# Kernel optimization log

Hardware: AMD Instinct MI355X
Metric: run time of the kernel (lower is better)

Reference implementation:

```python
import jax, jax.numpy as jnp
import numpy as np

D = 512       # hidden_size (attention defaults hardcode 512)
N = 8         # num_heads
H = D // N    # depth per head = 64
FF = 2048     # FFN filter size (hardcoded)
EPS = 1e-6


def _layer_norm(x, gamma, beta):
    # matches functional layer_norm: biased variance, eps inside sqrt
    mean = jnp.mean(x, axis=-1, keepdims=True)
    var = jnp.mean((x - mean) ** 2, axis=-1, keepdims=True)
    return gamma * ((x - mean) / jnp.sqrt(var + EPS)) + beta


def setup_inputs() -> dict:
    key = jax.random.key(0)
    ks = jax.random.split(key, 12)
    B, S = 8, 1024
    s = lambda k, shape, scale: jax.random.normal(k, shape, jnp.float32) * scale
    return {
        "inputs": s(ks[0], (B, S, D), 1.0),
        "attention_bias": jnp.zeros((B, 1, 1, S), jnp.float32),
        "ln1_g": jnp.ones((D,), jnp.float32),
        "ln1_b": jnp.zeros((D,), jnp.float32),
        "wq": s(ks[1], (D, N, H), D ** -0.5),
        "wk": s(ks[2], (D, N, H), D ** -0.5),
        "wv": s(ks[3], (D, N, H), D ** -0.5),
        "wo": s(ks[4], (N, H, D), D ** -0.5),
        "ln2_g": jnp.ones((D,), jnp.float32),
        "ln2_b": jnp.zeros((D,), jnp.float32),
        "w1": s(ks[5], (D, FF), D ** -0.5),
        "b1": jnp.zeros((FF,), jnp.float32),
        "w2": s(ks[6], (FF, D), FF ** -0.5),
        "b2": jnp.zeros((D,), jnp.float32),
    }


def reference(inputs, attention_bias, ln1_g, ln1_b, wq, wk, wv, wo,
              ln2_g, ln2_b, w1, b1, w2, b2):
    # --- self-attention block (pre-LN, residual) ---
    y = _layer_norm(inputs, ln1_g, ln1_b)
    q = jnp.einsum('bsd,dnh->bsnh', y, wq) * (H ** -0.5)
    k = jnp.einsum('bsd,dnh->bsnh', y, wk)
    v = jnp.einsum('bsd,dnh->bsnh', y, wv)
    # logits[b,n,f,t] = sum_h k[b,t,n,h] * q[b,f,n,h]
    logits = jnp.einsum('btnh,bfnh->bnft', k, q) + attention_bias
    weights = jax.nn.softmax(logits, axis=3)
    attn = jnp.einsum('bnft,btnh->bfnh', weights, v)
    attn_out = jnp.einsum('bfnh,nhd->bfd', attn, wo)
    x = inputs + attn_out

    # --- FFN block (pre-LN, residual) ---
    y2 = _layer_norm(x, ln2_g, ln2_b)
    h = jax.nn.relu(jnp.einsum('bsd,df->bsf', y2, w1) + b1)
    ffn_out = jnp.einsum('bsf,fd->bsd', h, w2) + b2
    return x + ffn_out
```

## Files before the change

### kernel.cpp

```cpp
#include <hip/hip_runtime.h>
#include <stdint.h>

typedef unsigned short u16;
typedef __attribute__((ext_vector_type(8))) __bf16 bf16x8;
typedef __attribute__((ext_vector_type(2))) __bf16 bf16x2;
typedef __attribute__((ext_vector_type(4))) float f32x4;

__device__ __forceinline__ float bf2f(u16 u) {
    union { unsigned int i; float f; } c; c.i = ((unsigned int)u) << 16; return c.f;
}
__device__ __forceinline__ u16 f2bf_sw(float f) {
    union { float f; unsigned int i; } c; c.f = f;
    unsigned int u = c.i;
    u += 0x7FFFu + ((u >> 16) & 1u);
    return (u16)(u >> 16);
}
__device__ __forceinline__ unsigned f2bf2(float lo, float hi) {
#if __has_builtin(__builtin_amdgcn_cvt_pk_bf16_f32)
    union { bf16x2 v; unsigned u; } c;
    c.v = __builtin_amdgcn_cvt_pk_bf16_f32(lo, hi);
    return c.u;
#else
    return (unsigned)f2bf_sw(lo) | ((unsigned)f2bf_sw(hi) << 16);
#endif
}
__device__ __forceinline__ u16 f2bf(float f) {
#if __has_builtin(__builtin_amdgcn_cvt_pk_bf16_f32)
    return (u16)(f2bf2(f, 0.f) & 0xFFFFu);
#else
    return f2bf_sw(f);
#endif
}
__device__ __forceinline__ bool sniff_f32(const unsigned* probe) {
    return probe && ((*probe & 0xFFFFu) == 0u);
}
__device__ __forceinline__ float lde(const void* p, size_t i, bool isf32) {
    return isf32 ? ((const float*)p)[i] : bf2f(((const u16*)p)[i]);
}
__device__ __forceinline__ void g2lds16(const void* g, void* l) {
    __builtin_amdgcn_global_load_lds(
        (__attribute__((address_space(1))) void*)(uintptr_t)g,
        (__attribute__((address_space(3))) void*)(unsigned int)(uintptr_t)l,
        16, 0, 0);
}

__global__ void prep_weights(const void* __restrict__ wq, const void* __restrict__ wk,
                             const void* __restrict__ wv, const void* __restrict__ wo,
                             const void* __restrict__ w1, const void* __restrict__ w2,
                             u16* __restrict__ wqkvT, u16* __restrict__ woT,
                             u16* __restrict__ w1T, u16* __restrict__ w2T,
                             const unsigned* probe) {
    __shared__ u16 t[32][33];
    const bool isf32 = sniff_f32(probe);
    const int id = blockIdx.x;
    const void* src; u16* dst; int R, C, cb, rb; float scale = 1.f;
    if (id < 1024) {
        const int which = id >> 8, tl = id & 255;
        R = 512; C = 512; cb = (tl & 15) * 32; rb = (tl >> 4) * 32;
        if (which == 0)      { src = wq; dst = wqkvT;              scale = 0.18033688011112042f; }
        else if (which == 1) { src = wk; dst = wqkvT + 512 * 512; }
        else if (which == 2) { src = wv; dst = wqkvT + 1024 * 512; }
        else                 { src = wo; dst = woT; }
    } else if (id < 2048) {
        const int tl = id - 1024; src = w1; dst = w1T; R = 512; C = 2048;
        cb = (tl & 63) * 32; rb = (tl >> 6) * 32;
    } else {
        const int tl = id - 2048; src = w2; dst = w2T; R = 2048; C = 512;
        cb = (tl & 15) * 32; rb = (tl >> 4) * 32;
    }
    const int tx = threadIdx.x, ty = threadIdx.y;
#pragma unroll
    for (int i = 0; i < 4; i++)
        t[ty + i * 8][tx] = f2bf(lde(src, (size_t)(rb + ty + i * 8) * C + cb + tx, isf32));
    __syncthreads();
#pragma unroll
    for (int i = 0; i < 4; i++) {
        float v = bf2f(t[tx][ty + i * 8]) * scale;
        dst[(size_t)(cb + ty + i * 8) * R + rb + tx] = f2bf(v);
    }
}

__global__ __launch_bounds__(256) void ln_any(const void* __restrict__ x,
                                              const void* __restrict__ gw,
                                              const void* __restrict__ bw,
                                              u16* __restrict__ y,
                                              const unsigned* probe_x,
                                              const unsigned* probe_gb) {
    const bool xf32 = sniff_f32(probe_x);
    const bool gf32 = sniff_f32(probe_gb);
    const int lane = threadIdx.x & 63, wave = threadIdx.x >> 6;
    const int r = blockIdx.x * 4 + wave;
    union U8 { uint4 v; u16 s[8]; };
    float xs[8];
    if (xf32) {
        const float4* xr = (const float4*)((const float*)x + (size_t)r * 512 + lane * 8);
        float4 p0 = xr[0], p1 = xr[1];
        xs[0]=p0.x; xs[1]=p0.y; xs[2]=p0.z; xs[3]=p0.w;
        xs[4]=p1.x; xs[5]=p1.y; xs[6]=p1.z; xs[7]=p1.w;
    } else {
        U8 xu; xu.v = *(const uint4*)((const u16*)x + (size_t)r * 512 + lane * 8);
#pragma unroll
        for (int j = 0; j < 8; j++) xs[j] = bf2f(xu.s[j]);
    }
    float s1 = 0.f, s2 = 0.f;
#pragma unroll
    for (int j = 0; j < 8; j++) { s1 += xs[j]; s2 += xs[j] * xs[j]; }
#pragma unroll
    for (int d = 1; d < 64; d <<= 1) { s1 += __shfl_xor(s1, d); s2 += __shfl_xor(s2, d); }
    const float mean = s1 * (1.f / 512.f);
    const float var = s2 * (1.f / 512.f) - mean * mean;
    const float rstd = rsqrtf(var + 1e-6f);
    float gs[8], bs[8];
    if (gf32) {
        const float4* gr = (const float4*)((const float*)gw + lane * 8);
        const float4* br = (const float4*)((const float*)bw + lane * 8);
        float4 g0 = gr[0], g1 = gr[1], b0 = br[0], b1 = br[1];
        gs[0]=g0.x; gs[1]=g0.y; gs[2]=g0.z; gs[3]=g0.w; gs[4]=g1.x; gs[5]=g1.y; gs[6]=g1.z; gs[7]=g1.w;
        bs[0]=b0.x; bs[1]=b0.y; bs[2]=b0.z; bs[3]=b0.w; bs[4]=b1.x; bs[5]=b1.y; bs[6]=b1.z; bs[7]=b1.w;
    } else {
        U8 gu; gu.v = *(const uint4*)((const u16*)gw + lane * 8);
        U8 bu; bu.v = *(const uint4*)((const u16*)bw + lane * 8);
#pragma unroll
        for (int j = 0; j < 8; j++) { gs[j] = bf2f(gu.s[j]); bs[j] = bf2f(bu.s[j]); }
    }
    uint4 ov;
    float o[8];
#pragma unroll
    for (int j = 0; j < 8; j++) o[j] = gs[j] * ((xs[j] - mean) * rstd) + bs[j];
    ov.x = f2bf2(o[0], o[1]); ov.y = f2bf2(o[2], o[3]);
    ov.z = f2bf2(o[4], o[5]); ov.w = f2bf2(o[6], o[7]);
    *(uint4*)(y + (size_t)r * 512 + lane * 8) = ov;
}

template <int EPI, int TM>
__global__ __launch_bounds__(256, 2) void gemm_bt(const u16* __restrict__ A,
                                                  const u16* __restrict__ Bt,
                                                  const void* __restrict__ bias,
                                                  const void* __restrict__ res,
                                                  void* __restrict__ out,
                                                  u16* __restrict__ out2,
                                                  const unsigned* probe,
                                                  int M, int N, int K) {
    constexpr int ACH = TM / 16;
    constexpr int MI = TM / 32;
    __shared__ __align__(16) u16 lA[2][TM * 32];
    __shared__ __align__(16) u16 lB[2][128 * 32];
    const int tid = threadIdx.x, wave = tid >> 6, lane = tid & 63;
    const int m0 = blockIdx.x * TM, n0 = blockIdx.y * 128;
    const int wm = (wave >> 1) * (TM / 2), wn = (wave & 1) * 64;
    const int row = lane & 15, quad = lane >> 4;
    f32x4 acc[MI][4];
#pragma unroll
    for (int i = 0; i < MI; i++)
#pragma unroll
        for (int j = 0; j < 4; j++) acc[i][j] = (f32x4){0.f, 0.f, 0.f, 0.f};
    const u16* Ab = A + (size_t)m0 * K;
    const u16* Bb = Bt + (size_t)n0 * K;

    auto stage = [&](int buf, int k0) {
#pragma unroll
        for (int c = 0; c < (ACH + 8 + 3) / 4; c++) {
            const int ch = c * 4 + wave;
            if (ch < ACH) {
                const int e = ch * 64 + lane;
                const int r = e >> 2, col = (e & 3) * 8;
                g2lds16(Ab + (size_t)r * K + k0 + col, (char*)lA[buf] + ch * 1024);
            } else if (ch < ACH + 8) {
                const int c2 = ch - ACH;
                const int e = c2 * 64 + lane;
                const int r = e >> 2, col = (e & 3) * 8;
                g2lds16(Bb + (size_t)r * K + k0 + col, (char*)lB[buf] + c2 * 1024);
            }
        }
    };

    stage(0, 0);
    int cur = 0;
    for (int k0 = 0; k0 < K; k0 += 32) {
        __syncthreads();
        if (k0 + 32 < K) stage(cur ^ 1, k0 + 32);
        bf16x8 af[MI], bfr[4];
#pragma unroll
        for (int t = 0; t < MI; t++)
            af[t]  = *(const bf16x8*)(lA[cur] + (wm + t * 16 + row) * 32 + quad * 8);
#pragma unroll
        for (int t = 0; t < 4; t++)
            bfr[t] = *(const bf16x8*)(lB[cur] + (wn + t * 16 + row) * 32 + quad * 8);
#pragma unroll
        for (int i = 0; i < MI; i++)
#pragma unroll
            for (int j = 0; j < 4; j++)
                acc[i][j] = __builtin_amdgcn_mfma_f32_16x16x32_bf16(af[i], bfr[j], acc[i][j], 0, 0, 0);
        cur ^= 1;
    }
    const bool isf32 = sniff_f32(probe);
#pragma unroll
    for (int i = 0; i < MI; i++) {
        const int gm = m0 + wm + i * 16 + quad * 4;
#pragma unroll
        for (int j = 0; j < 4; j++) {
            const int gn = n0 + wn + j * 16 + row;
            float bv = 0.f;
            if (EPI == 2 || EPI == 3) bv = lde(bias, gn, isf32);
#pragma unroll
            for (int r = 0; r < 4; r++) {
                float v = acc[i][j][r];
                const int gmr = gm + r;
                size_t idx = (size_t)gmr * N + gn;
                if (EPI == 1) {
                    ((u16*)out)[idx] = f2bf(v + lde(res, idx, isf32));
                } else if (EPI == 2) {
                    v += bv;
                    ((u16*)out)[idx] = f2bf(v > 0.f ? v : 0.f);
                } else if (EPI == 3) {
                    v += bv + bf2f(((const u16*)res)[idx]);
                    if (isf32) ((float*)out)[idx] = v;
                    else       ((u16*)out)[idx] = f2bf(v);
                } else {
                    if (gn < 1024) {
                        ((u16*)out)[(size_t)gmr * 1024 + gn] = f2bf(v);
                    } else {
                        const int j2 = gn - 1024, n = j2 >> 6, h2 = j2 & 63;
                        const int b = gmr >> 10, t = gmr & 1023;
                        const int ut = t & 31, vt = ut & 15;
                        const int tP = (t & ~31) | ((vt >> 2) * 8 + ((ut >> 4) << 2) + (vt & 3));
                        out2[(((size_t)b * 8 + n) * 64 + h2) * 1024 + tP] = f2bf(v);
                    }
                }
            }
        }
    }
}

__global__ __launch_bounds__(256, 4) void attn_fused(const u16* __restrict__ qk,
                                                     const u16* __restrict__ vT,
                                                     const void* __restrict__ biasp,
                                                     u16* __restrict__ attn,
                                                     const unsigned* probe) {
    __shared__ __align__(16) u16 lQ[64 * 64];
    __shared__ __align__(16) u16 lK[2][64 * 64];
    __shared__ __align__(16) u16 lV[2][64 * 64];
    const bool isf32 = sniff_f32(probe);
    const int tid = threadIdx.x, wave = tid >> 6, lane = tid & 63;
    const int row = lane & 15, quad = lane >> 4;
    const int r7 = row & 7;
    const int g0 = (quad ^ r7) * 8;
    const int bn = blockIdx.x, b = bn >> 3, n = bn & 7;
    const int f0 = blockIdx.y * 64;
    const u16* Qg = qk + (size_t)(b * 1024 + f0) * 1024 + n * 64;
    const u16* Kg = qk + (size_t)(b * 1024) * 1024 + 512 + n * 64;
    const u16* Vg = vT + (size_t)bn * 65536;

#pragma unroll
    for (int j = 0; j < 2; j++) {
        const int ch = wave * 2 + j, e = ch * 64 + lane;
        const int rq = e >> 3, cq = ((e & 7) ^ (rq & 7)) * 8;
        g2lds16(Qg + (size_t)rq * 1024 + cq, (char*)lQ + ch * 1024);
    }

    auto stage = [&](int buf, int t0) {
#pragma unroll
        for (int j = 0; j < 4; j++) {
            const int ch = wave * 4 + j;
            if (ch < 8) {
                const int e = ch * 64 + lane;
                const int rk = e >> 3, ck = ((e & 7) ^ (rk & 7)) * 8;
                g2lds16(Kg + (size_t)(t0 + rk) * 1024 + ck, (char*)&lK[buf][0] + ch * 1024);
            } else {
                const int e = (ch - 8) * 64 + lane;
                const int rv = e >> 3, cv = ((e & 7) ^ (rv & 7)) * 8;
                g2lds16(Vg + (size_t)rv * 1024 + t0 + cv, (char*)&lV[buf][0] + (ch - 8) * 1024);
            }
        }
    };

    stage(0, 0);
    __syncthreads();

    const int fr = wave * 16 + row;
    bf16x8 bq[2];
#pragma unroll
    for (int ks = 0; ks < 2; ks++)
        bq[ks] = *(const bf16x8*)(lQ + fr * 64 + (g0 ^ (ks * 32)));

    float l_i = 0.f;
    f32x4 oacc[4];
#pragma unroll
    for (int h = 0; h < 4; h++) oacc[h] = (f32x4){0.f, 0.f, 0.f, 0.f};

    auto compute = [&](int buf, int t0) {
        float bv4[4][4];
#pragma unroll
        for (int nt = 0; nt < 4; nt++) {
            const size_t bidx = (size_t)b * 1024 + t0 + nt * 16 + quad * 4;
            if (isf32) {
                float4 t4 = *(const float4*)((const float*)biasp + bidx);
                bv4[nt][0] = t4.x; bv4[nt][1] = t4.y; bv4[nt][2] = t4.z; bv4[nt][3] = t4.w;
            } else {
                union { uint2 v; u16 s[4]; } bu;
                bu.v = *(const uint2*)((const u16*)biasp + bidx);
#pragma unroll
                for (int r = 0; r < 4; r++) bv4[nt][r] = bf2f(bu.s[r]);
            }
        }
        f32x4 s[4];
#pragma unroll
        for (int nt = 0; nt < 4; nt++) s[nt] = (f32x4){0.f, 0.f, 0.f, 0.f};
#pragma unroll
        for (int nt = 0; nt < 4; nt++) {
#pragma unroll
            for (int ks = 0; ks < 2; ks++) {
                bf16x8 ak = *(const bf16x8*)(&lK[buf][0] + (nt * 16 + row) * 64 + (g0 ^ (ks * 32)));
                s[nt] = __builtin_amdgcn_mfma_f32_16x16x32_bf16(ak, bq[ks], s[nt], 0, 0, 0);
            }
        }
#pragma unroll
        for (int nt = 0; nt < 4; nt++)
#pragma unroll
            for (int r = 0; r < 4; r++) {
                float p = __builtin_exp2f(fmaf(bv4[nt][r], 1.4426950408889634f, s[nt][r]));
                s[nt][r] = p;
                l_i += p;
            }
#pragma unroll
        for (int ks = 0; ks < 2; ks++) {
            union { unsigned u[4]; bf16x8 v8; } bb;
            bb.u[0] = f2bf2(s[ks * 2][0],     s[ks * 2][1]);
            bb.u[1] = f2bf2(s[ks * 2][2],     s[ks * 2][3]);
            bb.u[2] = f2bf2(s[ks * 2 + 1][0], s[ks * 2 + 1][1]);
            bb.u[3] = f2bf2(s[ks * 2 + 1][2], s[ks * 2 + 1][3]);
#pragma unroll
            for (int ht = 0; ht < 4; ht++) {
                bf16x8 av = *(const bf16x8*)(&lV[buf][0] + (ht * 16 + row) * 64 + (g0 ^ (ks * 32)));
                oacc[ht] = __builtin_amdgcn_mfma_f32_16x16x32_bf16(av, bb.v8, oacc[ht], 0, 0, 0);
            }
        }
    };

    for (int t0 = 0; t0 < 1024; t0 += 128) {
        __syncthreads();
        stage(1, t0 + 64);
        compute(0, t0);
        __syncthreads();
        if (t0 + 128 < 1024) stage(0, t0 + 128);
        compute(1, t0 + 64);
    }

    l_i += __shfl_xor(l_i, 16);
    l_i += __shfl_xor(l_i, 32);
    const float inv = 1.f / l_i;
    const int f = f0 + wave * 16 + row;
#pragma unroll
    for (int ht = 0; ht < 4; ht++) {
        uint2 ov;
        ov.x = f2bf2(oacc[ht][0] * inv, oacc[ht][1] * inv);
        ov.y = f2bf2(oacc[ht][2] * inv, oacc[ht][3] * inv);
        *(uint2*)(attn + (size_t)(b * 1024 + f) * 512 + n * 64 + ht * 16 + quad * 4) = ov;
    }
}

extern "C" void kernel_launch(void* const* d_in, const int* in_sizes, int n_in,
                              void* d_out, int out_size, void* d_ws, size_t ws_size,
                              hipStream_t stream) {
    const void* inp  = d_in[0];
    const void* ab   = d_in[1];
    const void* ln1g = d_in[2];
    const void* ln1b = d_in[3];
    const void* wq   = d_in[4];
    const void* wk   = d_in[5];
    const void* wv   = d_in[6];
    const void* wo   = d_in[7];
    const void* ln2g = d_in[8];
    const void* ln2b = d_in[9];
    const void* w1   = d_in[10];
    const void* b1   = d_in[11];
    const void* w2   = d_in[12];
    const void* b2   = d_in[13];
    const unsigned* probe = (const unsigned*)d_in[2];

    char* ws = (char*)d_ws;
    size_t off = 0;
    auto alloc = [&](size_t bytes) -> void* { void* p = ws + off; off += bytes; return p; };
    u16* wqkvT = (u16*)alloc(1536 * 512 * 2);
    u16* woT   = (u16*)alloc(512 * 512 * 2);
    u16* w1T   = (u16*)alloc(2048 * 512 * 2);
    u16* w2T   = (u16*)alloc(512 * 2048 * 2);
    u16* ybuf  = (u16*)alloc((size_t)8192 * 512 * 2);
    u16* qk    = (u16*)alloc((size_t)8192 * 1024 * 2);
    u16* vT    = (u16*)alloc((size_t)64 * 64 * 1024 * 2);
    u16* attn  = (u16*)alloc((size_t)8192 * 512 * 2);
    u16* xbf   = (u16*)alloc((size_t)8192 * 512 * 2);
    u16* hbuf  = qk;

    prep_weights<<<3072, dim3(32, 8), 0, stream>>>(wq, wk, wv, wo, w1, w2,
                                                   wqkvT, woT, w1T, w2T, probe);
    ln_any<<<2048, 256, 0, stream>>>(inp, ln1g, ln1b, ybuf, probe, probe);
    gemm_bt<4, 128><<<dim3(64, 12), 256, 0, stream>>>(ybuf, wqkvT, nullptr, nullptr, qk, vT, nullptr, 8192, 1536, 512);
    attn_fused<<<dim3(64, 16), 256, 0, stream>>>(qk, vT, ab, attn, probe);
    gemm_bt<1, 64><<<dim3(128, 4), 256, 0, stream>>>(attn, woT, nullptr, inp, xbf, nullptr, probe, 8192, 512, 512);
    ln_any<<<2048, 256, 0, stream>>>(xbf, ln2g, ln2b, ybuf, nullptr, probe);
    gemm_bt<2, 128><<<dim3(64, 16), 256, 0, stream>>>(ybuf, w1T, b1, nullptr, hbuf, nullptr, probe, 8192, 2048, 512);
    gemm_bt<3, 64><<<dim3(128, 4), 256, 0, stream>>>(hbuf, w2T, b2, xbf, (u16*)d_out, nullptr, probe, 8192, 512, 2048);
}
```

Before: 251.3 us.

## Restructure attention K/V pipeline with explicit vmcnt waits and LDS-staged bias

Rewrites the attention main loop as a double-buffered pipeline that prefetches two tiles ahead, using explicit s_waitcnt vmcnt counts and raw s_barrier with sched_barrier fences in place of __syncthreads. The attention bias row is staged into LDS once, reusing the Q buffer after Q is moved to registers, instead of being read from global memory on every tile. The goal is to keep more loads in flight and cut full memory drains at each barrier. The hand-counted vmcnt values and barrier placement are fragile and can produce races if the load counts per wave are wrong.

Result: no change. 252.2 us (+0.4%).

```diff
diff --git a/kernel.cpp b/kernel.cpp
--- a/kernel.cpp
+++ b/kernel.cpp
@@ -42,6 +42,11 @@
         (__attribute__((address_space(1))) void*)(uintptr_t)g,
         (__attribute__((address_space(3))) void*)(unsigned int)(uintptr_t)l,
         16, 0, 0);
+}
+__device__ __forceinline__ void fence_bar() {
+    __builtin_amdgcn_sched_barrier(0);
+    __builtin_amdgcn_s_barrier();
+    __builtin_amdgcn_sched_barrier(0);
 }
 
 __global__ void prep_weights(const void* __restrict__ wq, const void* __restrict__ wk,
@@ -243,22 +248,14 @@
     const bool isf32 = sniff_f32(probe);
     const int tid = threadIdx.x, wave = tid >> 6, lane = tid & 63;
     const int row = lane & 15, quad = lane >> 4;
-    const int r7 = row & 7;
-    const int g0 = (quad ^ r7) * 8;
+    const int g0 = (quad ^ (row & 7)) * 8;
     const int bn = blockIdx.x, b = bn >> 3, n = bn & 7;
     const int f0 = blockIdx.y * 64;
     const u16* Qg = qk + (size_t)(b * 1024 + f0) * 1024 + n * 64;
     const u16* Kg = qk + (size_t)(b * 1024) * 1024 + 512 + n * 64;
     const u16* Vg = vT + (size_t)bn * 65536;
 
-#pragma unroll
-    for (int j = 0; j < 2; j++) {
-        const int ch = wave * 2 + j, e = ch * 64 + lane;
-        const int rq = e >> 3, cq = ((e & 7) ^ (rq & 7)) * 8;
-        g2lds16(Qg + (size_t)rq * 1024 + cq, (char*)lQ + ch * 1024);
-    }
-
-    auto stage = [&](int buf, int t0) {
+    auto stageKV = [&](int buf, int t0) {
 #pragma unroll
         for (int j = 0; j < 4; j++) {
             const int ch = wave * 4 + j;
@@ -274,14 +271,33 @@
         }
     };
 
-    stage(0, 0);
-    __syncthreads();
+#pragma unroll
+    for (int j = 0; j < 2; j++) {
+        const int ch = wave * 2 + j, e = ch * 64 + lane;
+        const int rq = e >> 3, cq = ((e & 7) ^ (rq & 7)) * 8;
+        g2lds16(Qg + (size_t)rq * 1024 + cq, (char*)lQ + ch * 1024);
+    }
+    stageKV(0, 0);
+    asm volatile("s_waitcnt vmcnt(0)" ::: "memory");
+    fence_bar();
 
     const int fr = wave * 16 + row;
     bf16x8 bq[2];
-#pragma unroll
-    for (int ks = 0; ks < 2; ks++)
-        bq[ks] = *(const bf16x8*)(lQ + fr * 64 + (g0 ^ (ks * 32)));
+    bq[0] = *(const bf16x8*)(lQ + fr * 64 + g0);
+    bq[1] = *(const bf16x8*)(lQ + fr * 64 + (g0 ^ 32));
+    asm volatile("s_waitcnt lgkmcnt(0)" ::: "memory");
+    fence_bar();
+
+    if (isf32) {
+        g2lds16((const float*)biasp + (size_t)b * 1024 + wave * 256 + lane * 4,
+                (char*)lQ + wave * 1024);
+    } else if (wave < 2) {
+        g2lds16((const u16*)biasp + (size_t)b * 1024 + wave * 512 + lane * 8,
+                (char*)lQ + wave * 1024);
+    }
+    stageKV(1, 64);
+    asm volatile("s_waitcnt vmcnt(4)" ::: "memory");
+    fence_bar();
 
     float l_i = 0.f;
     f32x4 oacc[4];
@@ -289,39 +305,37 @@
     for (int h = 0; h < 4; h++) oacc[h] = (f32x4){0.f, 0.f, 0.f, 0.f};
 
     auto compute = [&](int buf, int t0) {
-        float bv4[4][4];
+        f32x4 s[4];
+#pragma unroll
+        for (int nt = 0; nt < 4; nt++) s[nt] = (f32x4){0.f, 0.f, 0.f, 0.f};
 #pragma unroll
         for (int nt = 0; nt < 4; nt++) {
-            const size_t bidx = (size_t)b * 1024 + t0 + nt * 16 + quad * 4;
+            const int tr = nt * 16 + row;
+            bf16x8 ak0 = *(const bf16x8*)(&lK[buf][0] + tr * 64 + g0);
+            s[nt] = __builtin_amdgcn_mfma_f32_16x16x32_bf16(ak0, bq[0], s[nt], 0, 0, 0);
+            bf16x8 ak1 = *(const bf16x8*)(&lK[buf][0] + tr * 64 + (g0 ^ 32));
+            s[nt] = __builtin_amdgcn_mfma_f32_16x16x32_bf16(ak1, bq[1], s[nt], 0, 0, 0);
+        }
+#pragma unroll
+        for (int nt = 0; nt < 4; nt++) {
+            const int tl = t0 + nt * 16 + quad * 4;
+            float bv4[4];
             if (isf32) {
-                float4 t4 = *(const float4*)((const float*)biasp + bidx);
-                bv4[nt][0] = t4.x; bv4[nt][1] = t4.y; bv4[nt][2] = t4.z; bv4[nt][3] = t4.w;
+                float4 t4 = *(const float4*)((const float*)lQ + tl);
+                bv4[0] = t4.x; bv4[1] = t4.y; bv4[2] = t4.z; bv4[3] = t4.w;
             } else {
                 union { uint2 v; u16 s[4]; } bu;
-                bu.v = *(const uint2*)((const u16*)biasp + bidx);
-#pragma unroll
-                for (int r = 0; r < 4; r++) bv4[nt][r] = bf2f(bu.s[r]);
-            }
-        }
-        f32x4 s[4];
-#pragma unroll
-        for (int nt = 0; nt < 4; nt++) s[nt] = (f32x4){0.f, 0.f, 0.f, 0.f};
-#pragma unroll
-        for (int nt = 0; nt < 4; nt++) {
-#pragma unroll
-            for (int ks = 0; ks < 2; ks++) {
-                bf16x8 ak = *(const bf16x8*)(&lK[buf][0] + (nt * 16 + row) * 64 + (g0 ^ (ks * 32)));
-                s[nt] = __builtin_amdgcn_mfma_f32_16x16x32_bf16(ak, bq[ks], s[nt], 0, 0, 0);
-            }
-        }
-#pragma unroll
-        for (int nt = 0; nt < 4; nt++)
+                bu.v = *(const uint2*)((const u16*)lQ + tl);
+#pragma unroll
+                for (int r = 0; r < 4; r++) bv4[r] = bf2f(bu.s[r]);
+            }
 #pragma unroll
             for (int r = 0; r < 4; r++) {
-                float p = __builtin_exp2f(fmaf(bv4[nt][r], 1.4426950408889634f, s[nt][r]));
+                float p = __builtin_exp2f(fmaf(bv4[r], 1.4426950408889634f, s[nt][r]));
                 s[nt][r] = p;
                 l_i += p;
             }
+        }
 #pragma unroll
         for (int ks = 0; ks < 2; ks++) {
             union { unsigned u[4]; bf16x8 v8; } bb;
@@ -337,14 +351,21 @@
         }
     };
 
-    for (int t0 = 0; t0 < 1024; t0 += 128) {
-        __syncthreads();
-        stage(1, t0 + 64);
-        compute(0, t0);
-        __syncthreads();
-        if (t0 + 128 < 1024) stage(0, t0 + 128);
-        compute(1, t0 + 64);
-    }
+    int cur = 0;
+#pragma unroll 1
+    for (int i = 0; i < 15; i++) {
+        compute(cur, i * 64);
+        fence_bar();
+        if (i <= 13) {
+            stageKV(cur, (i + 2) * 64);
+            asm volatile("s_waitcnt vmcnt(4)" ::: "memory");
+        } else {
+            asm volatile("s_waitcnt vmcnt(0)" ::: "memory");
+        }
+        fence_bar();
+        cur ^= 1;
+    }
+    compute(cur, 15 * 64);
 
     l_i += __shfl_xor(l_i, 16);
     l_i += __shfl_xor(l_i, 32);
```
